# Performance work log

Measured on AMD Instinct MI355X. Metric: run time of the kernel, lower is better.

## Reference

```python
import jax, jax.numpy as jnp
import numpy as np

D_MODEL = 1024
N_HEADS = 16
D_K = D_MODEL // N_HEADS
THETA = 10000.0
NEG_INF = -1e30


def _rope_tables(token_positions, d_k, theta=THETA):
    # freqs[t, i] = t / theta**(2i/d_k), i in [0, d_k/2)
    exponent = jnp.arange(0, d_k, 2, dtype=jnp.float32)  # [d_k/2]
    inv_freq = 1.0 / theta ** (exponent / d_k)
    freqs = token_positions.astype(jnp.float32)[:, None] * inv_freq[None, :]  # [s, d_k/2]
    return jnp.cos(freqs), jnp.sin(freqs)


def _apply_rope(x, cos, sin):
    # x: [..., s, d_k]; interleaved pair rotation (pairs are (x[2i], x[2i+1]))
    x1 = x[..., 0::2]
    x2 = x[..., 1::2]
    r1 = x1 * cos - x2 * sin
    r2 = x1 * sin + x2 * cos
    return jnp.stack([r1, r2], axis=-1).reshape(x.shape)


def setup_inputs() -> dict:
    key = jax.random.key(0)
    ks = jax.random.split(key, 5)
    b, s = 2, 2048
    scale = np.sqrt(2.0 / (D_MODEL + D_MODEL))
    return {
        "x": jax.random.normal(ks[0], (b, s, D_MODEL), dtype=jnp.float32),
        "Wq": jax.random.normal(ks[1], (D_MODEL, D_MODEL), dtype=jnp.float32) * scale,
        "Wk": jax.random.normal(ks[2], (D_MODEL, D_MODEL), dtype=jnp.float32) * scale,
        "Wv": jax.random.normal(ks[3], (D_MODEL, D_MODEL), dtype=jnp.float32) * scale,
        "Wo": jax.random.normal(ks[4], (D_MODEL, D_MODEL), dtype=jnp.float32) * scale,
        "token_positions": jnp.arange(s, dtype=jnp.int64 if jax.config.jax_enable_x64 else jnp.int32),
    }


def reference(x, Wq, Wk, Wv, Wo, token_positions):
    b, s, _ = x.shape
    # QKV projections: weight stored [in, out]
    q = jnp.einsum('bsi,io->bso', x, Wq)
    k = jnp.einsum('bsi,io->bso', x, Wk)
    v = jnp.einsum('bsi,io->bso', x, Wv)
    # split heads: [b, h, s, d_k]
    q = q.reshape(b, s, N_HEADS, D_K).transpose(0, 2, 1, 3)
    k = k.reshape(b, s, N_HEADS, D_K).transpose(0, 2, 1, 3)
    v = v.reshape(b, s, N_HEADS, D_K).transpose(0, 2, 1, 3)
    # RoPE
    cos, sin = _rope_tables(token_positions, D_K)
    q = _apply_rope(q, cos, sin)
    k = _apply_rope(k, cos, sin)
    # causal attention with full materialized scores (faithful to source)
    scores = jnp.einsum('bhid,bhjd->bhij', q, k) / jnp.sqrt(jnp.float32(D_K))
    mask = jnp.tril(jnp.ones((s, s), dtype=bool))
    scores = jnp.where(mask, scores, NEG_INF)
    probs = jax.nn.softmax(scores, axis=-1)
    out = jnp.einsum('bhij,bhjd->bhid', probs, v)
    out = out.transpose(0, 2, 1, 3).reshape(b, s, D_MODEL)
    return jnp.einsum('bsi,io->bso', out, Wo)
```

## Files before the change

kernel.cpp:

```cpp
#include <hip/hip_runtime.h>
#include <hip/hip_bf16.h>
#include <cmath>

#define S_LEN 2048
#define DMODEL 1024
#define NHEADS 16
#define DK 64
#define BATCH 2
#define MTOT (BATCH * S_LEN)

using short8 = __attribute__((ext_vector_type(8))) short;
using floatx4 = __attribute__((ext_vector_type(4))) float;

__device__ __forceinline__ unsigned short f2b(float f) {
    union { float f; unsigned u; } v; v.f = f;
    unsigned r = v.u + 0x7fff + ((v.u >> 16) & 1);
    return (unsigned short)(r >> 16);
}

__device__ __forceinline__ unsigned pack2(float a, float b) {
    float2 t; t.x = a; t.y = b;
    __hip_bfloat162 h = __float22bfloat162_rn(t);
    union { __hip_bfloat162 h; unsigned u; } v; v.h = h;
    return v.u;
}

__device__ __forceinline__ void gload16(const void* g, void* l) {
    __builtin_amdgcn_global_load_lds(
        (const __attribute__((address_space(1))) unsigned int*)g,
        (__attribute__((address_space(3))) unsigned int*)l, 16, 0, 0);
}

#define FENCE() asm volatile("" ::: "memory")

__global__ __launch_bounds__(256) void prep_k(
    const float* __restrict__ x, unsigned short* __restrict__ xb,
    const int* __restrict__ tokpos, float* __restrict__ ct, float* __restrict__ st,
    const float* W0, const float* W1, const float* W2, const float* W3,
    unsigned short* T0, unsigned short* T1, unsigned short* T2, unsigned short* T3) {
    __shared__ float t[64][65];
    const int b = blockIdx.x;
    if (b < 2048) {
        int i = (b * 256 + threadIdx.x) * 8;
        float4 a = *(const float4*)(x + i);
        float4 bb = *(const float4*)(x + i + 4);
        short8 o;
        o[0] = f2b(a.x); o[1] = f2b(a.y); o[2] = f2b(a.z); o[3] = f2b(a.w);
        o[4] = f2b(bb.x); o[5] = f2b(bb.y); o[6] = f2b(bb.z); o[7] = f2b(bb.w);
        *(short8*)(xb + i) = o;
    } else if (b < 2304) {
        int idx = (b - 2048) * 256 + threadIdx.x;
        int si = idx >> 5;
        int ip = idx & 31;
        float pos = (float)tokpos[si];
        float inv_freq = powf(10000.0f, -(float)(2 * ip) / 64.0f);
        float ang = pos * inv_freq;
        ct[idx] = cosf(ang);
        st[idx] = sinf(ang);
    } else {
        int id = b - 2304;
        int z = id >> 8;
        int bx = id & 15, by = (id >> 4) & 15;
        const float* W = z == 0 ? W0 : z == 1 ? W1 : z == 2 ? W2 : W3;
        unsigned short* T = z == 0 ? T0 : z == 1 ? T1 : z == 2 ? T2 : T3;
        const bool perm = (z < 2);
        int n0 = bx * 64, k0 = by * 64;
        int rr = threadIdx.x >> 6, cc = threadIdx.x & 63;
#pragma unroll
        for (int r = 0; r < 16; r++) {
            int row = r * 4 + rr;
            t[row][cc] = W[(size_t)(k0 + row) * DMODEL + n0 + cc];
        }
        __syncthreads();
#pragma unroll
        for (int r = 0; r < 16; r++) {
            int row = r * 4 + rr;
            int drow = perm ? (((row & 1) ? 32 : 0) + (row >> 1)) : row;
            T[(size_t)(n0 + drow) * DMODEL + k0 + cc] = f2b(t[cc][row]);
        }
    }
}

__global__ __launch_bounds__(256) void zero_k(float* __restrict__ p) {
    int i = (blockIdx.x * 256 + threadIdx.x) * 4;
    *(float4*)(p + i) = (float4){0.f, 0.f, 0.f, 0.f};
}

__global__ __launch_bounds__(256) void vtrans_k(const unsigned short* __restrict__ V,
                                                unsigned short* __restrict__ Vt) {
    __shared__ unsigned short t[64][72];
    const int tid = threadIdx.x;
    const int s0 = blockIdx.x * 64, d0 = blockIdx.y * 64;
    const int bb = s0 >> 11;
#pragma unroll
    for (int it = 0; it < 4; it++) {
        int e = (it * 256 + tid) * 4;
        int r = e >> 6, c = e & 63;
        *(ushort4*)&t[r][c] = *(const ushort4*)(V + (size_t)(s0 + r) * DMODEL + d0 + c);
    }
    __syncthreads();
#pragma unroll
    for (int it = 0; it < 4; it++) {
        int e = (it * 256 + tid) * 4;
        int r = e >> 6, c = e & 63;
        ushort4 v;
        v.x = t[c + 0][r]; v.y = t[c + 1][r];
        v.z = t[c + 2][r]; v.w = t[c + 3][r];
        *(ushort4*)(Vt + (size_t)(bb * 1024 + d0 + r) * S_LEN + (s0 & (S_LEN - 1)) + c) = v;
    }
}

__global__ __launch_bounds__(512, 2) void mm_k(
    const unsigned short* __restrict__ A,
    const unsigned short* __restrict__ Bt0, const unsigned short* __restrict__ Bt1,
    const unsigned short* __restrict__ Bt2,
    void* C0, void* C1, void* C2,
    const float* __restrict__ ct, const float* __restrict__ st, int kind) {
    __shared__ __align__(16) unsigned short blob[10 * 8192];

    const int z = blockIdx.z;
    const unsigned short* Bt = (kind == 1) ? Bt0 : (z == 0 ? Bt0 : z == 1 ? Bt1 : Bt2);
    void* C = (kind == 1) ? C0 : (z == 0 ? C0 : z == 1 ? C1 : C2);
    const int mode = (kind == 1) ? 0 : (z == 2 ? 3 : 1);
    const int t0 = (kind == 1) ? z * 4 : 0;
    const int NT = (kind == 1) ? 4 : 16;
    const float qscale = (z == 0 && kind == 0) ? 0.18033688011112042f : 1.0f;

    const int tid = threadIdx.x;
    const int w = tid >> 6, lane = tid & 63;
    const int l15 = lane & 15, quad = lane >> 4;
    const int wr = w >> 2, wc = w & 3;
    const int m0 = blockIdx.x * 256, n0 = blockIdx.y * 256;

    const int rbase = (w >> 1) * 16 + l15;
    const int cbase = (w & 1) * 32 + quad * 8;

    floatx4 acc[8][4];
#pragma unroll
    for (int i = 0; i < 8; i++)
#pragma unroll
        for (int j = 0; j < 4; j++) acc[i][j] = (floatx4){0.f, 0.f, 0.f, 0.f};

    auto stage_half = [&](int h) {
        const int ts = t0 + (h >> 2), part = h & 3;
        const int slot = h % 10;
        const unsigned short* src =
            (part < 2 ? A + (((size_t)(m0 + part * 128 + rbase)) << 10)
                      : Bt + (((size_t)(n0 + (part - 2) * 128 + rbase)) << 10))
            + (size_t)ts * 64 + cbase;
        char* d = (char*)blob + slot * 16384 + w * 1024;
        gload16(src, d);
        gload16(src + (64 << 10), d + 8192);
    };

#pragma unroll
    for (int h = 0; h < 6; ++h) stage_half(h);
    asm volatile("s_waitcnt vmcnt(4)" ::: "memory");
    FENCE(); __builtin_amdgcn_s_barrier(); FENCE();

    short8 af[4][2];
    for (int t = 0; t < NT; ++t) {
        const int sb = (4 * t) % 10;
        int sA = sb + wr;            if (sA >= 10) sA -= 10;
        int sB = sb + 2 + (wc >> 1); if (sB >= 10) sB -= 10;
        const char* LA = (const char*)blob + sA * 16384;
        const char* LB = (const char*)blob + sB * 16384;
#pragma unroll
        for (int q = 0; q < 4; ++q) {
            const int rh = q >> 1, ch = q & 1;
            if (ch == 0) {
#pragma unroll
                for (int ii = 0; ii < 4; ++ii)
#pragma unroll
                    for (int kh = 0; kh < 2; ++kh)
                        af[ii][kh] = *(const short8*)(LA + ((rh * 4 + ii) * 2 + kh) * 1024 + lane * 16);
            }
            short8 bf[2][2];
#pragma unroll
            for (int jj = 0; jj < 2; ++jj)
#pragma unroll
                for (int kh = 0; kh < 2; ++kh)
                    bf[jj][kh] = *(const short8*)(LB + (((wc & 1) * 4 + ch * 2 + jj) * 2 + kh) * 1024 + lane * 16);
            const int h = 4 * t + q + 6;
            if (h < 4 * NT) stage_half(h);
            if (q == 3) {
                if (t == NT - 2) asm volatile("s_waitcnt vmcnt(0)" ::: "memory");
                else             asm volatile("s_waitcnt vmcnt(4)" ::: "memory");
            }
            FENCE(); __builtin_amdgcn_s_barrier(); FENCE();
            __builtin_amdgcn_s_setprio(1);
#pragma unroll
            for (int ii = 0; ii < 4; ++ii)
#pragma unroll
                for (int jj = 0; jj < 2; ++jj) {
                    floatx4 a0 = acc[rh * 4 + ii][ch * 2 + jj];
                    a0 = __builtin_amdgcn_mfma_f32_16x16x32_bf16(af[ii][0], bf[jj][0], a0, 0, 0, 0);
                    a0 = __builtin_amdgcn_mfma_f32_16x16x32_bf16(af[ii][1], bf[jj][1], a0, 0, 0, 0);
                    acc[rh * 4 + ii][ch * 2 + jj] = a0;
                }
            __builtin_amdgcn_s_setprio(0);
            FENCE(); __builtin_amdgcn_s_barrier(); FENCE();
        }
    }

#pragma unroll
    for (int i = 0; i < 8; i++) {
        const int rowb = m0 + wr * 128 + i * 16 + quad * 4;
        if (mode == 0) {
            float* Cf = (float*)C;
#pragma unroll
            for (int j = 0; j < 4; j++) {
                int colb = n0 + wc * 64 + j * 16 + l15;
#pragma unroll
                for (int r = 0; r < 4; r++)
                    unsafeAtomicAdd(&Cf[(size_t)(rowb + r) * DMODEL + colb], acc[i][j][r]);
            }
        } else if (mode == 1) {
            unsigned short* Cb = (unsigned short*)C;
#pragma unroll
            for (int jh = 0; jh < 2; jh++) {
                int ip = jh * 16 + l15;
                int cole = n0 + wc * 64 + jh * 16 + l15;
#pragma unroll
                for (int r = 0; r < 4; r++) {
                    int row = rowb + r;
                    int si = row & (S_LEN - 1);
                    float c = ct[si * 32 + ip] * qscale;
                    float s = st[si * 32 + ip] * qscale;
                    float e = acc[i][jh][r];
                    float od = acc[i][jh + 2][r];
                    Cb[(size_t)row * DMODEL + cole] = f2b(e * c - od * s);
                    Cb[(size_t)row * DMODEL + cole + 32] = f2b(e * s + od * c);
                }
            }
        } else {
            unsigned short* Cb = (unsigned short*)C;
#pragma unroll
            for (int j = 0; j < 4; j++) {
                int colb = n0 + wc * 64 + j * 16 + l15;
#pragma unroll
                for (int r = 0; r < 4; r++)
                    Cb[(size_t)(rowb + r) * DMODEL + colb] = f2b(acc[i][j][r]);
            }
        }
    }
}

__global__ __launch_bounds__(512) void attn_k(const unsigned short* __restrict__ Q,
                                              const unsigned short* __restrict__ K,
                                              const unsigned short* __restrict__ Vt,
                                              unsigned short* __restrict__ O) {
    __shared__ __align__(16) unsigned short Kblob[2][4096];
    __shared__ __align__(16) unsigned short Vblob[2][4096];
    __shared__ __align__(16) unsigned short Ps[8][16 * 72];

    const int tid = threadIdx.x;
    const int w = tid >> 6, lane = tid & 63;
    const int l15 = lane & 15, quad = lane >> 4;
    const int idx = blockIdx.x;
    const int qt = 15 - (idx >> 5);
    const int bh = idx & 31;
    const int bb = bh >> 4, h = bh & 15;
    const int qbase = qt * 128 + w * 16;
    const int qrow = qbase + l15;

    const size_t qoff = (size_t)(bb * S_LEN + qbase + l15) * DMODEL + h * DK;
    short8 aq0 = *(const short8*)(Q + qoff + quad * 8);
    short8 aq1 = *(const short8*)(Q + qoff + 32 + quad * 8);

    floatx4 o[4];
#pragma unroll
    for (int f = 0; f < 4; f++) o[f] = (floatx4){0.f, 0.f, 0.f, 0.f};
    float mv = -1e30f, lv = 0.f;

    const unsigned short* Kb = K + (size_t)(bb * S_LEN) * DMODEL + h * DK;
    const unsigned short* Vb = Vt + (size_t)(bb * 1024 + h * DK) * S_LEN;
    unsigned short* ps = &Ps[w][0];

    auto stage = [&](int b, int kb) {
#pragma unroll
        for (int it = 0; it < 2; it++) {
            int g = it * 8 + w;
            if (g < 8) {
                const unsigned short* gp =
                    Kb + (size_t)(kb + (g >> 1) * 16 + l15) * DMODEL + (g & 1) * 32 + quad * 8;
                gload16(gp, (char*)&Kblob[b][0] + g * 1024);
            } else {
                int gv = g - 8;
                const unsigned short* gp =
                    Vb + (size_t)((gv >> 1) * 16 + l15) * S_LEN + kb + (gv & 1) * 32 + quad * 8;
                gload16(gp, (char*)&Vblob[b][0] + gv * 1024);
            }
        }
    };

    const int nkt = 2 * qt + 2;
    stage(0, 0);
    for (int kt = 0; kt < nkt; kt++) {
        const int b = kt & 1;
        const int kb = kt * 64;
        __syncthreads();
        if (kt + 1 < nkt) stage(b ^ 1, (kt + 1) * 64);

        const unsigned short* kbb = &Kblob[b][0];
        floatx4 c[4];
#pragma unroll
        for (int g = 0; g < 4; g++) {
            short8 kf0 = *(const short8*)(kbb + (g * 2 + 0) * 512 + lane * 8);
            short8 kf1 = *(const short8*)(kbb + (g * 2 + 1) * 512 + lane * 8);
            floatx4 t = {0.f, 0.f, 0.f, 0.f};
            t = __builtin_amdgcn_mfma_f32_16x16x32_bf16(kf0, aq0, t, 0, 0, 0);
            c[g] = __builtin_amdgcn_mfma_f32_16x16x32_bf16(kf1, aq1, t, 0, 0, 0);
        }

        float sv[16];
        if (kb + 63 <= qbase) {
#pragma unroll
            for (int g = 0; g < 4; g++)
#pragma unroll
                for (int r = 0; r < 4; r++) sv[g * 4 + r] = c[g][r];
        } else {
#pragma unroll
            for (int g = 0; g < 4; g++)
#pragma unroll
                for (int r = 0; r < 4; r++) {
                    int key = kb + g * 16 + quad * 4 + r;
                    sv[g * 4 + r] = (key <= qrow) ? c[g][r] : -1e30f;
                }
        }
        float mx = sv[0];
#pragma unroll
        for (int i = 1; i < 16; i++) mx = fmaxf(mx, sv[i]);
        mx = fmaxf(mx, __shfl_xor(mx, 16));
        mx = fmaxf(mx, __shfl_xor(mx, 32));
        float mnew = fmaxf(mv, mx);
        float alpha = exp2f(mv - mnew);
        mv = mnew;
        float p[16], psum = 0.f;
#pragma unroll
        for (int i = 0; i < 16; i++) {
            p[i] = exp2f(sv[i] - mnew);
            psum += p[i];
        }
        lv = lv * alpha + psum;

#pragma unroll
        for (int g = 0; g < 4; g++) {
            uint2 pk;
            pk.x = pack2(p[g * 4 + 0], p[g * 4 + 1]);
            pk.y = pack2(p[g * 4 + 2], p[g * 4 + 3]);
            *(uint2*)(ps + l15 * 72 + g * 16 + quad * 4) = pk;
        }
#pragma unroll
        for (int f = 0; f < 4; f++) {
            o[f][0] *= alpha; o[f][1] *= alpha;
            o[f][2] *= alpha; o[f][3] *= alpha;
        }
        short8 pf0 = *(const short8*)(ps + l15 * 72 + quad * 8);
        short8 pf1 = *(const short8*)(ps + l15 * 72 + 32 + quad * 8);
        const unsigned short* vbb = &Vblob[b][0];
#pragma unroll
        for (int f = 0; f < 4; f++) {
            short8 vf0 = *(const short8*)(vbb + (f * 2 + 0) * 512 + lane * 8);
            short8 vf1 = *(const short8*)(vbb + (f * 2 + 1) * 512 + lane * 8);
            o[f] = __builtin_amdgcn_mfma_f32_16x16x32_bf16(vf0, pf0, o[f], 0, 0, 0);
            o[f] = __builtin_amdgcn_mfma_f32_16x16x32_bf16(vf1, pf1, o[f], 0, 0, 0);
        }
    }

    lv += __shfl_xor(lv, 16);
    lv += __shfl_xor(lv, 32);
    float inv = 1.0f / lv;
    __syncthreads();
#pragma unroll
    for (int f = 0; f < 4; f++) {
        uint2 pk;
        pk.x = pack2(o[f][0] * inv, o[f][1] * inv);
        pk.y = pack2(o[f][2] * inv, o[f][3] * inv);
        *(uint2*)(ps + l15 * 72 + f * 16 + quad * 4) = pk;
    }
    short8 r0 = *(const short8*)(ps + l15 * 72 + quad * 8);
    short8 r1 = *(const short8*)(ps + l15 * 72 + 32 + quad * 8);
    size_t obase = (size_t)(bb * S_LEN + qbase + l15) * DMODEL + h * DK;
    *(short8*)(O + obase + quad * 8) = r0;
    *(short8*)(O + obase + 32 + quad * 8) = r1;
}

extern "C" void kernel_launch(void* const* d_in, const int* in_sizes, int n_in,
                              void* d_out, int out_size, void* d_ws,
                              size_t ws_size, hipStream_t stream) {
    const float* x = (const float*)d_in[0];
    const float* Wq = (const float*)d_in[1];
    const float* Wk = (const float*)d_in[2];
    const float* Wv = (const float*)d_in[3];
    const float* Wo = (const float*)d_in[4];
    const int* tokpos = (const int*)d_in[5];
    float* out = (float*)d_out;

    const size_t MD = (size_t)MTOT * DMODEL;
    const size_t WD = (size_t)DMODEL * DMODEL;
    unsigned short* xb = (unsigned short*)d_ws;
    unsigned short* Wqt = xb + MD;
    unsigned short* Wkt = Wqt + WD;
    unsigned short* Wvt = Wkt + WD;
    unsigned short* Wot = Wvt + WD;
    unsigned short* Q = Wot + WD;
    unsigned short* K = Q + MD;
    unsigned short* V = K + MD;
    unsigned short* Vt = V + MD;
    float* ct = (float*)(Vt + MD);
    float* st = ct + S_LEN * 32;
    unsigned short* O = V;

    prep_k<<<dim3(3328), dim3(256), 0, stream>>>(x, xb, tokpos, ct, st,
                                                 Wq, Wk, Wv, Wo, Wqt, Wkt, Wvt, Wot);
    zero_k<<<dim3(4096), dim3(256), 0, stream>>>(out);

    mm_k<<<dim3(16, 4, 3), dim3(512), 0, stream>>>(xb, Wqt, Wkt, Wvt,
                                                   (void*)Q, (void*)K, (void*)V, ct, st, 0);
    vtrans_k<<<dim3(64, 16), dim3(256), 0, stream>>>(V, Vt);
    attn_k<<<dim3(512), dim3(512), 0, stream>>>(Q, K, Vt, O);
    mm_k<<<dim3(16, 4, 4), dim3(512), 0, stream>>>(O, Wot, Wot, Wot,
                                                   (void*)out, (void*)out, (void*)out, ct, st, 1);
}
```

Measured before the change: 242.4 us.

## Replace atomic split-K output GEMM with two partials plus add; skip masked attention tiles

```diff
diff --git a/kernel.cpp b/kernel.cpp
--- a/kernel.cpp
+++ b/kernel.cpp
@@ -81,9 +81,17 @@
     }
 }
 
-__global__ __launch_bounds__(256) void zero_k(float* __restrict__ p) {
-    int i = (blockIdx.x * 256 + threadIdx.x) * 4;
-    *(float4*)(p + i) = (float4){0.f, 0.f, 0.f, 0.f};
+__global__ __launch_bounds__(256) void add_k(float* __restrict__ out,
+                                             const float* __restrict__ p) {
+    int i = (blockIdx.x * 256 + threadIdx.x) * 8;
+    float4 a = *(const float4*)(out + i);
+    float4 b = *(const float4*)(p + i);
+    float4 c = *(const float4*)(out + i + 4);
+    float4 d = *(const float4*)(p + i + 4);
+    a.x += b.x; a.y += b.y; a.z += b.z; a.w += b.w;
+    c.x += d.x; c.y += d.y; c.z += d.z; c.w += d.w;
+    *(float4*)(out + i) = a;
+    *(float4*)(out + i + 4) = c;
 }
 
 __global__ __launch_bounds__(256) void vtrans_k(const unsigned short* __restrict__ V,
@@ -120,10 +128,10 @@
 
     const int z = blockIdx.z;
     const unsigned short* Bt = (kind == 1) ? Bt0 : (z == 0 ? Bt0 : z == 1 ? Bt1 : Bt2);
-    void* C = (kind == 1) ? C0 : (z == 0 ? C0 : z == 1 ? C1 : C2);
+    void* C = (kind == 1) ? (z == 0 ? C0 : C1) : (z == 0 ? C0 : z == 1 ? C1 : C2);
     const int mode = (kind == 1) ? 0 : (z == 2 ? 3 : 1);
-    const int t0 = (kind == 1) ? z * 4 : 0;
-    const int NT = (kind == 1) ? 4 : 16;
+    const int t0 = (kind == 1) ? z * 8 : 0;
+    const int NT = (kind == 1) ? 8 : 16;
     const float qscale = (z == 0 && kind == 0) ? 0.18033688011112042f : 1.0f;
 
     const int tid = threadIdx.x;
@@ -213,7 +221,7 @@
                 int colb = n0 + wc * 64 + j * 16 + l15;
 #pragma unroll
                 for (int r = 0; r < 4; r++)
-                    unsafeAtomicAdd(&Cf[(size_t)(rowb + r) * DMODEL + colb], acc[i][j][r]);
+                    Cf[(size_t)(rowb + r) * DMODEL + colb] = acc[i][j][r];
             }
         } else if (mode == 1) {
             unsigned short* Cb = (unsigned short*)C;
@@ -302,69 +310,82 @@
         __syncthreads();
         if (kt + 1 < nkt) stage(b ^ 1, (kt + 1) * 64);
 
-        const unsigned short* kbb = &Kblob[b][0];
-        floatx4 c[4];
-#pragma unroll
-        for (int g = 0; g < 4; g++) {
-            short8 kf0 = *(const short8*)(kbb + (g * 2 + 0) * 512 + lane * 8);
-            short8 kf1 = *(const short8*)(kbb + (g * 2 + 1) * 512 + lane * 8);
-            floatx4 t = {0.f, 0.f, 0.f, 0.f};
-            t = __builtin_amdgcn_mfma_f32_16x16x32_bf16(kf0, aq0, t, 0, 0, 0);
-            c[g] = __builtin_amdgcn_mfma_f32_16x16x32_bf16(kf1, aq1, t, 0, 0, 0);
-        }
-
-        float sv[16];
-        if (kb + 63 <= qbase) {
-#pragma unroll
-            for (int g = 0; g < 4; g++)
-#pragma unroll
-                for (int r = 0; r < 4; r++) sv[g * 4 + r] = c[g][r];
-        } else {
-#pragma unroll
-            for (int g = 0; g < 4; g++)
-#pragma unroll
-                for (int r = 0; r < 4; r++) {
-                    int key = kb + g * 16 + quad * 4 + r;
-                    sv[g * 4 + r] = (key <= qrow) ? c[g][r] : -1e30f;
+        if (kb <= qbase + 15) {
+            const unsigned short* kbb = &Kblob[b][0];
+            floatx4 c[4];
+            __builtin_amdgcn_s_setprio(1);
+#pragma unroll
+            for (int g = 0; g < 4; g++) {
+                short8 kf0 = *(const short8*)(kbb + (g * 2 + 0) * 512 + lane * 8);
+                short8 kf1 = *(const short8*)(kbb + (g * 2 + 1) * 512 + lane * 8);
+                floatx4 t = {0.f, 0.f, 0.f, 0.f};
+                t = __builtin_amdgcn_mfma_f32_16x16x32_bf16(kf0, aq0, t, 0, 0, 0);
+                c[g] = __builtin_amdgcn_mfma_f32_16x16x32_bf16(kf1, aq1, t, 0, 0, 0);
+            }
+            __builtin_amdgcn_s_setprio(0);
+
+            float sv[16];
+            if (kb + 63 <= qbase) {
+#pragma unroll
+                for (int g = 0; g < 4; g++)
+#pragma unroll
+                    for (int r = 0; r < 4; r++) sv[g * 4 + r] = c[g][r];
+            } else {
+#pragma unroll
+                for (int g = 0; g < 4; g++)
+#pragma unroll
+                    for (int r = 0; r < 4; r++) {
+                        int key = kb + g * 16 + quad * 4 + r;
+                        sv[g * 4 + r] = (key <= qrow) ? c[g][r] : -1e30f;
+                    }
+            }
+            float t0 = fmaxf(fmaxf(sv[0], sv[1]), sv[2]);
+            float t1 = fmaxf(fmaxf(sv[3], sv[4]), sv[5]);
+            float t2 = fmaxf(fmaxf(sv[6], sv[7]), sv[8]);
+            float t3 = fmaxf(fmaxf(sv[9], sv[10]), sv[11]);
+            float t4 = fmaxf(fmaxf(sv[12], sv[13]), sv[14]);
+            float mx = fmaxf(fmaxf(fmaxf(t0, t1), fmaxf(t2, t3)), fmaxf(t4, sv[15]));
+            mx = fmaxf(mx, __shfl_xor(mx, 16));
+            mx = fmaxf(mx, __shfl_xor(mx, 32));
+
+            if (!__all(mx <= mv)) {
+                float mnew = fmaxf(mv, mx);
+                float alpha = exp2f(mv - mnew);
+                mv = mnew;
+                lv *= alpha;
+#pragma unroll
+                for (int f = 0; f < 4; f++) {
+                    o[f][0] *= alpha; o[f][1] *= alpha;
+                    o[f][2] *= alpha; o[f][3] *= alpha;
                 }
-        }
-        float mx = sv[0];
-#pragma unroll
-        for (int i = 1; i < 16; i++) mx = fmaxf(mx, sv[i]);
-        mx = fmaxf(mx, __shfl_xor(mx, 16));
-        mx = fmaxf(mx, __shfl_xor(mx, 32));
-        float mnew = fmaxf(mv, mx);
-        float alpha = exp2f(mv - mnew);
-        mv = mnew;
-        float p[16], psum = 0.f;
-#pragma unroll
-        for (int i = 0; i < 16; i++) {
-            p[i] = exp2f(sv[i] - mnew);
-            psum += p[i];
-        }
-        lv = lv * alpha + psum;
-
-#pragma unroll
-        for (int g = 0; g < 4; g++) {
-            uint2 pk;
-            pk.x = pack2(p[g * 4 + 0], p[g * 4 + 1]);
-            pk.y = pack2(p[g * 4 + 2], p[g * 4 + 3]);
-            *(uint2*)(ps + l15 * 72 + g * 16 + quad * 4) = pk;
-        }
-#pragma unroll
-        for (int f = 0; f < 4; f++) {
-            o[f][0] *= alpha; o[f][1] *= alpha;
-            o[f][2] *= alpha; o[f][3] *= alpha;
-        }
-        short8 pf0 = *(const short8*)(ps + l15 * 72 + quad * 8);
-        short8 pf1 = *(const short8*)(ps + l15 * 72 + 32 + quad * 8);
-        const unsigned short* vbb = &Vblob[b][0];
-#pragma unroll
-        for (int f = 0; f < 4; f++) {
-            short8 vf0 = *(const short8*)(vbb + (f * 2 + 0) * 512 + lane * 8);
-            short8 vf1 = *(const short8*)(vbb + (f * 2 + 1) * 512 + lane * 8);
-            o[f] = __builtin_amdgcn_mfma_f32_16x16x32_bf16(vf0, pf0, o[f], 0, 0, 0);
-            o[f] = __builtin_amdgcn_mfma_f32_16x16x32_bf16(vf1, pf1, o[f], 0, 0, 0);
+            }
+            float p[16], psum = 0.f;
+#pragma unroll
+            for (int i = 0; i < 16; i++) {
+                p[i] = exp2f(sv[i] - mv);
+                psum += p[i];
+            }
+            lv += psum;
+
+#pragma unroll
+            for (int g = 0; g < 4; g++) {
+                uint2 pk;
+                pk.x = pack2(p[g * 4 + 0], p[g * 4 + 1]);
+                pk.y = pack2(p[g * 4 + 2], p[g * 4 + 3]);
+                *(uint2*)(ps + l15 * 72 + g * 16 + quad * 4) = pk;
+            }
+            short8 pf0 = *(const short8*)(ps + l15 * 72 + quad * 8);
+            short8 pf1 = *(const short8*)(ps + l15 * 72 + 32 + quad * 8);
+            const unsigned short* vbb = &Vblob[b][0];
+            __builtin_amdgcn_s_setprio(1);
+#pragma unroll
+            for (int f = 0; f < 4; f++) {
+                short8 vf0 = *(const short8*)(vbb + (f * 2 + 0) * 512 + lane * 8);
+                short8 vf1 = *(const short8*)(vbb + (f * 2 + 1) * 512 + lane * 8);
+                o[f] = __builtin_amdgcn_mfma_f32_16x16x32_bf16(vf0, pf0, o[f], 0, 0, 0);
+                o[f] = __builtin_amdgcn_mfma_f32_16x16x32_bf16(vf1, pf1, o[f], 0, 0, 0);
+            }
+            __builtin_amdgcn_s_setprio(0);
         }
     }
 
@@ -411,15 +432,16 @@
     float* ct = (float*)(Vt + MD);
     float* st = ct + S_LEN * 32;
     unsigned short* O = V;
+    float* P1 = (float*)Q;
 
     prep_k<<<dim3(3328), dim3(256), 0, stream>>>(x, xb, tokpos, ct, st,
                                                  Wq, Wk, Wv, Wo, Wqt, Wkt, Wvt, Wot);
-    zero_k<<<dim3(4096), dim3(256), 0, stream>>>(out);
 
     mm_k<<<dim3(16, 4, 3), dim3(512), 0, stream>>>(xb, Wqt, Wkt, Wvt,
                                                    (void*)Q, (void*)K, (void*)V, ct, st, 0);
     vtrans_k<<<dim3(64, 16), dim3(256), 0, stream>>>(V, Vt);
     attn_k<<<dim3(512), dim3(512), 0, stream>>>(Q, K, Vt, O);
-    mm_k<<<dim3(16, 4, 4), dim3(512), 0, stream>>>(O, Wot, Wot, Wot,
-                                                   (void*)out, (void*)out, (void*)out, ct, st, 1);
-}
+    mm_k<<<dim3(16, 4, 2), dim3(512), 0, stream>>>(O, Wot, Wot, Wot,
+                                                   (void*)out, (void*)P1, (void*)P1, ct, st, 1);
+    add_k<<<dim3(2048), dim3(256), 0, stream>>>(out, P1);
+}
```

Measured after the change: 211.2 us. 1.15x faster.
